# Performance work log

Measured on AMD Instinct MI355X. Metric: run time of the kernel, lower is better.

## Reference

```python
import jax, jax.numpy as jnp
import numpy as np

CHUNK = 2048  # query chunk for KNN to avoid materializing full NxN distance matrix


def _knn_single(pos, k):
    # pos: [N,3] -> idx [N,k] of k nearest neighbors (incl. self)
    N = pos.shape[0]
    qs = pos.reshape(N // CHUNK, CHUNK, 3)

    def per_chunk(q):
        d = jnp.sum((q[:, None, :] - pos[None, :, :]) ** 2, axis=-1)  # [CHUNK,N]
        _, idx = jax.lax.top_k(-d, k)
        return idx

    return jax.lax.map(per_chunk, qs).reshape(N, k)


def setup_inputs() -> dict:
    key = jax.random.key(0)
    ks = jax.random.split(key, 8)
    B, N, Cin, Cout, H, K = 2, 16384, 32, 64, 128, 16
    Ein = 2 * Cin + 3  # in_feat + out(self)_feat + rel_pos

    def lin(k_, fi, fo):
        return jax.random.normal(k_, (fi, fo), jnp.float32) / np.sqrt(fi)

    return dict(
        positions=jax.random.uniform(ks[0], (B, N, 3), jnp.float32),
        features=jax.random.normal(ks[1], (B, N, Cin), jnp.float32),
        W1=lin(ks[2], Ein, H), b1=jnp.zeros((H,), jnp.float32),
        W2=lin(ks[3], H, Cout), b2=jnp.zeros((Cout,), jnp.float32),
        W3=lin(ks[4], Cout, H), b3=jnp.zeros((H,), jnp.float32),
        W4=lin(ks[5], H, Cout), b4=jnp.zeros((Cout,), jnp.float32),
        knn_k=K,
    )


def reference(positions, features, W1, b1, W2, b2, W3, b3, W4, b4, knn_k):
    # 1) KNN neighbor search per batch
    idx = jax.vmap(lambda p: _knn_single(p, knn_k))(positions)  # [B,N,K]
    gather = jax.vmap(lambda a, i: a[i])
    # 2) gather neighbor features / positions
    nbr_feat = gather(features, idx)                      # [B,N,K,Cin]
    nbr_pos = gather(positions, idx)                      # [B,N,K,3]
    rel_pos = nbr_pos - positions[:, :, None, :]          # [B,N,K,3]
    self_feat = jnp.broadcast_to(features[:, :, None, :], nbr_feat.shape)
    # 3) edge features: cat(in_feat, out_feat, rel_pos)
    edge = jnp.concatenate([nbr_feat, self_feat, rel_pos], axis=-1)  # [B,N,K,Ein]
    # 4) edge MLP
    h = jax.nn.gelu(edge @ W1 + b1) @ W2 + b2             # [B,N,K,Cout]
    # 5) mean reduction over neighbors
    agg = jnp.mean(h, axis=2)                             # [B,N,Cout]
    # 6) output MLP
    return jax.nn.gelu(agg @ W3 + b3) @ W4 + b4           # [B,N,Cout]
```

## Files before the change

### kernel.cpp

```cpp
#include <hip/hip_runtime.h>
#include <math.h>

#define N_PTS 16384
#define BATCH 2
#define CIN   32
#define H_DIM 128
#define COUT  64
#define KNN   16
#define GC    16
#define NCELL (GC * GC * GC)
#define CS    (1.0f / GC)
#define PB    4
#define CHUNK 2048

typedef unsigned short ushortT;

__device__ __forceinline__ float gelu_f(float x) {
    float x3 = x * x * x;
    float t  = tanhf(0.7978845608028654f * (x + 0.044715f * x3));
    return 0.5f * x * (1.0f + t);
}
__device__ __forceinline__ float gelu_fast(float x) {
    float z = 1.5957691216057308f * (x + 0.044715f * x * x * x);
    return x / (1.0f + __expf(-z));
}

__device__ __forceinline__ int cellco(float v) {
    int c = (int)(v * (float)GC);
    return c < 0 ? 0 : (c > GC - 1 ? GC - 1 : c);
}

__global__ __launch_bounds__(256)
void zero_kernel(int* __restrict__ cnt) {
    cnt[blockIdx.x * 256 + threadIdx.x] = 0;
}

__global__ __launch_bounds__(256)
void count_kernel(const float* __restrict__ pos, int* __restrict__ cnt) {
    const int t = blockIdx.x * 256 + threadIdx.x;
    const int b = t >> 14;
    float x = pos[(size_t)t * 3 + 0];
    float y = pos[(size_t)t * 3 + 1];
    float z = pos[(size_t)t * 3 + 2];
    int cell = (cellco(z) * GC + cellco(y)) * GC + cellco(x);
    atomicAdd(&cnt[b * NCELL + cell], 1);
}

__global__ __launch_bounds__(1024)
void scan_kernel(const int* __restrict__ cnt, int* __restrict__ off,
                 int* __restrict__ cur) {
    __shared__ int s[1024];
    const int b = blockIdx.x;
    const int t = threadIdx.x;
    const int* c = cnt + b * NCELL;
    const int base = t * 4;
    int v0 = c[base], v1 = c[base + 1], v2 = c[base + 2], v3 = c[base + 3];
    int s01 = v0 + v1, s012 = s01 + v2, tot = s012 + v3;
    s[t] = tot;
    __syncthreads();
    for (int d = 1; d < 1024; d <<= 1) {
        int add = (t >= d) ? s[t - d] : 0;
        __syncthreads();
        s[t] += add;
        __syncthreads();
    }
    int excl = s[t] - tot;
    int* ob = off + b * (NCELL + 1);
    int* cb = cur + b * NCELL;
    ob[base] = excl;            cb[base] = excl;
    ob[base + 1] = excl + v0;   cb[base + 1] = excl + v0;
    ob[base + 2] = excl + s01;  cb[base + 2] = excl + s01;
    ob[base + 3] = excl + s012; cb[base + 3] = excl + s012;
    if (t == 1023) ob[NCELL] = excl + tot;
}

__global__ __launch_bounds__(256)
void scatter_kernel(const float* __restrict__ pos, int* __restrict__ cur,
                    float4* __restrict__ pos4) {
    const int t = blockIdx.x * 256 + threadIdx.x;
    const int b = t >> 14;
    const int pid = t & (N_PTS - 1);
    float x = pos[(size_t)t * 3 + 0];
    float y = pos[(size_t)t * 3 + 1];
    float z = pos[(size_t)t * 3 + 2];
    int cell = (cellco(z) * GC + cellco(y)) * GC + cellco(x);
    int slot = atomicAdd(&cur[b * NCELL + cell], 1);
    pos4[(size_t)b * N_PTS + slot] = make_float4(x, y, z, __int_as_float(pid));
}

__global__ __launch_bounds__(64)
void knnq_kernel(const float4* __restrict__ pos4,
                 const int* __restrict__ off, ushortT* __restrict__ out_idx) {
    const int t = blockIdx.x * 64 + threadIdx.x;
    const int b = t >> 14;
    const float4 Q = pos4[t];
    const float qx = Q.x, qy = Q.y, qz = Q.z;
    const int pid = __float_as_int(Q.w);
    const int cx = cellco(qx), cy = cellco(qy), cz = cellco(qz);
    const float4* p4b = pos4 + (size_t)b * N_PTS;
    const int* offb = off + b * (NCELL + 1);

    float ld[KNN]; int li[KNN];
#pragma unroll
    for (int p = 0; p < KNN; ++p) { ld[p] = 3.0e38f; li[p] = 0x7fffffff; }
    float t15d = 3.0e38f; int t15i = 0x7fffffff;

    auto scan_range = [&](int s, int e2) {
        for (int u = s; u < e2; u += 8) {
            float4 pg[8];
#pragma unroll
            for (int i = 0; i < 8; ++i) {
                int uu = u + i; uu = uu < e2 - 1 ? uu : e2 - 1;
                pg[i] = p4b[uu];
            }
#pragma unroll
            for (int i = 0; i < 8; ++i) {
                if (u + i >= e2) break;
                float ddx = __fsub_rn(qx, pg[i].x);
                float ddy = __fsub_rn(qy, pg[i].y);
                float ddz = __fsub_rn(qz, pg[i].z);
                float d = __fadd_rn(__fadd_rn(__fmul_rn(ddx, ddx),
                                              __fmul_rn(ddy, ddy)),
                                    __fmul_rn(ddz, ddz));
                int pj = __float_as_int(pg[i].w);
                if (d < t15d || (d == t15d && pj < t15i)) {
                    float cd = d; int cj = pj;
#pragma unroll
                    for (int p = 0; p < KNN; ++p) {
                        bool sw = (cd < ld[p]) || (cd == ld[p] && cj < li[p]);
                        float td = ld[p]; int ti = li[p];
                        ld[p] = sw ? cd : td; li[p] = sw ? cj : ti;
                        cd = sw ? td : cd;    cj = sw ? ti : cj;
                    }
                    t15d = ld[KNN - 1]; t15i = li[KNN - 1];
                }
            }
        }
    };

    for (int r = 1; r <= GC; ++r) {
        for (int dz = -r; dz <= r; ++dz) {
            const int Z = cz + dz; if ((unsigned)Z >= GC) continue;
            for (int dy = -r; dy <= r; ++dy) {
                const int Y = cy + dy; if ((unsigned)Y >= GC) continue;
                const int rowbase = (Z * GC + Y) * GC;
                const bool fullrow = (r == 1) ||
                    (dz == -r || dz == r || dy == -r || dy == r);
                if (fullrow) {
                    int X0 = cx - r; X0 = X0 < 0 ? 0 : X0;
                    int X1 = cx + r; X1 = X1 > GC - 1 ? GC - 1 : X1;
                    scan_range(offb[rowbase + X0], offb[rowbase + X1 + 1]);
                } else {
                    const int Xl = cx - r, Xr = cx + r;
                    if (Xl >= 0)
                        scan_range(offb[rowbase + Xl], offb[rowbase + Xl + 1]);
                    if (Xr <= GC - 1)
                        scan_range(offb[rowbase + Xr], offb[rowbase + Xr + 1]);
                }
            }
        }
        float mg = 1.0e19f;
        if (cx - r > 0)      mg = fminf(mg, qx - (float)(cx - r) * CS);
        if (cx + r < GC - 1) mg = fminf(mg, (float)(cx + r + 1) * CS - qx);
        if (cy - r > 0)      mg = fminf(mg, qy - (float)(cy - r) * CS);
        if (cy + r < GC - 1) mg = fminf(mg, (float)(cy + r + 1) * CS - qy);
        if (cz - r > 0)      mg = fminf(mg, qz - (float)(cz - r) * CS);
        if (cz + r < GC - 1) mg = fminf(mg, (float)(cz + r + 1) * CS - qz);
        if (t15d < mg * mg * 0.99999f) break;
    }
    ushortT* dst = out_idx + ((size_t)(b << 14) + pid) * KNN;
#pragma unroll
    for (int p = 0; p < KNN; ++p) dst[p] = (ushortT)li[p];
}

__global__ __launch_bounds__(256)
void feat1_kernel(const float* __restrict__ feats, const float* __restrict__ W1,
                  float* __restrict__ feat1) {
    const int g = blockIdx.x * 256 + threadIdx.x;
    const int p = g >> 7;
    const int h = g & 127;
    const float* fr = feats + (size_t)p * CIN;
    float a = 0.f;
#pragma unroll
    for (int c = 0; c < CIN; ++c)
        a += fr[c] * W1[c * H_DIM + h];
    feat1[g] = a;
}

__global__ __launch_bounds__(64)
void mlp2_kernel(const float* __restrict__ pos, const float* __restrict__ feats,
                 const ushortT* __restrict__ knn_idx, const float* __restrict__ feat1,
                 const float* __restrict__ W1, const float* __restrict__ b1,
                 const float* __restrict__ W2, const float* __restrict__ b2,
                 const float* __restrict__ W3, const float* __restrict__ b3,
                 const float* __restrict__ W4, const float* __restrict__ b4,
                 float* __restrict__ out) {
    __shared__ ushortT sIdx[PB][KNN];
    __shared__ float sq[PB][3];
    __shared__ __align__(16) float fself[PB][CIN];
    __shared__ float npx[PB][KNN][3];
    __shared__ __align__(16) float gs[PB][H_DIM];
    __shared__ __align__(16) float aggs[PB][COUT];
    __shared__ __align__(16) float hs[PB][H_DIM];

    const int tid = threadIdx.x;
    const int h0 = tid, h1 = tid + 64;
    const int i0 = blockIdx.x * PB;
    const size_t bofs = (size_t)(i0 >> 14) * N_PTS;

    for (int e = tid; e < PB * KNN; e += 64)
        sIdx[e >> 4][e & 15] = knn_idx[(size_t)(i0 + (e >> 4)) * KNN + (e & 15)];
    for (int e = tid; e < PB * 3; e += 64)
        sq[e / 3][e % 3] = pos[(size_t)(i0 + e / 3) * 3 + (e % 3)];
    for (int e = tid; e < PB * CIN; e += 64)
        fself[e >> 5][e & 31] = feats[(size_t)(i0 + (e >> 5)) * CIN + (e & 31)];
    __syncthreads();
    for (int e = tid; e < PB * KNN * 3; e += 64) {
        int p = e / (KNN * 3), r = e % (KNN * 3), k = r / 3, c = r % 3;
        npx[p][k][c] = pos[(bofs + sIdx[p][k]) * 3 + c];
    }

    const float w0A = W1[(2 * CIN + 0) * H_DIM + h0], w0B = W1[(2 * CIN + 0) * H_DIM + h1];
    const float w1A = W1[(2 * CIN + 1) * H_DIM + h0], w1B = W1[(2 * CIN + 1) * H_DIM + h1];
    const float w2A = W1[(2 * CIN + 2) * H_DIM + h0], w2B = W1[(2 * CIN + 2) * H_DIM + h1];
    float bA[PB], bB[PB];
#pragma unroll
    for (int p = 0; p < PB; ++p) { bA[p] = b1[h0]; bB[p] = b1[h1]; }
    __syncthreads();
#pragma unroll
    for (int c = 0; c < CIN; ++c) {
        float wA = W1[(CIN + c) * H_DIM + h0];
        float wB = W1[(CIN + c) * H_DIM + h1];
#pragma unroll
        for (int p = 0; p < PB; ++p) {
            bA[p] += fself[p][c] * wA;
            bB[p] += fself[p][c] * wB;
        }
    }

    float accA[PB] = {0.f, 0.f, 0.f, 0.f};
    float accB[PB] = {0.f, 0.f, 0.f, 0.f};
    for (int k = 0; k < KNN; ++k) {
#pragma unroll
        for (int p = 0; p < PB; ++p) {
            const float* fr = feat1 + (bofs + sIdx[p][k]) * H_DIM;
            float rx = npx[p][k][0] - sq[p][0];
            float ry = npx[p][k][1] - sq[p][1];
            float rz = npx[p][k][2] - sq[p][2];
            float uA = bA[p] + fr[h0] + rx * w0A + ry * w1A + rz * w2A;
            float uB = bB[p] + fr[h1] + rx * w0B + ry * w1B + rz * w2B;
            accA[p] += gelu_fast(uA);
            accB[p] += gelu_fast(uB);
        }
    }
#pragma unroll
    for (int p = 0; p < PB; ++p) {
        gs[p][h0] = accA[p] * (1.0f / KNN);
        gs[p][h1] = accB[p] * (1.0f / KNN);
    }
    __syncthreads();

    float a2[PB];
#pragma unroll
    for (int p = 0; p < PB; ++p) a2[p] = b2[h0];
    for (int c4 = 0; c4 < H_DIM / 4; ++c4) {
        float wx = W2[(4 * c4 + 0) * COUT + h0];
        float wy = W2[(4 * c4 + 1) * COUT + h0];
        float wz = W2[(4 * c4 + 2) * COUT + h0];
        float ww = W2[(4 * c4 + 3) * COUT + h0];
#pragma unroll
        for (int p = 0; p < PB; ++p) {
            float4 g = ((const float4*)gs[p])[c4];
            a2[p] += g.x * wx + g.y * wy + g.z * wz + g.w * ww;
        }
    }
#pragma unroll
    for (int p = 0; p < PB; ++p) aggs[p][h0] = a2[p];
    __syncthreads();

    float a3A[PB], a3B[PB];
#pragma unroll
    for (int p = 0; p < PB; ++p) { a3A[p] = b3[h0]; a3B[p] = b3[h1]; }
    for (int c4 = 0; c4 < COUT / 4; ++c4) {
        float wxA = W3[(4 * c4 + 0) * H_DIM + h0], wxB = W3[(4 * c4 + 0) * H_DIM + h1];
        float wyA = W3[(4 * c4 + 1) * H_DIM + h0], wyB = W3[(4 * c4 + 1) * H_DIM + h1];
        float wzA = W3[(4 * c4 + 2) * H_DIM + h0], wzB = W3[(4 * c4 + 2) * H_DIM + h1];
        float wwA = W3[(4 * c4 + 3) * H_DIM + h0], wwB = W3[(4 * c4 + 3) * H_DIM + h1];
#pragma unroll
        for (int p = 0; p < PB; ++p) {
            float4 g = ((const float4*)aggs[p])[c4];
            a3A[p] += g.x * wxA + g.y * wyA + g.z * wzA + g.w * wwA;
            a3B[p] += g.x * wxB + g.y * wyB + g.z * wzB + g.w * wwB;
        }
    }
#pragma unroll
    for (int p = 0; p < PB; ++p) {
        hs[p][h0] = gelu_fast(a3A[p]);
        hs[p][h1] = gelu_fast(a3B[p]);
    }
    __syncthreads();

    float o4[PB];
#pragma unroll
    for (int p = 0; p < PB; ++p) o4[p] = b4[h0];
    for (int c4 = 0; c4 < H_DIM / 4; ++c4) {
        float wx = W4[(4 * c4 + 0) * COUT + h0];
        float wy = W4[(4 * c4 + 1) * COUT + h0];
        float wz = W4[(4 * c4 + 2) * COUT + h0];
        float ww = W4[(4 * c4 + 3) * COUT + h0];
#pragma unroll
        for (int p = 0; p < PB; ++p) {
            float4 v = ((const float4*)hs[p])[c4];
            o4[p] += v.x * wx + v.y * wy + v.z * wz + v.w * ww;
        }
    }
#pragma unroll
    for (int p = 0; p < PB; ++p)
        out[(size_t)(i0 + p) * COUT + h0] = o4[p];
}

__global__ __launch_bounds__(64)
void mlp_kernel(const float* __restrict__ pos, const float* __restrict__ feats,
                const ushortT* __restrict__ knn_idx,
                const float* __restrict__ W1, const float* __restrict__ b1,
                const float* __restrict__ W2, const float* __restrict__ b2,
                const float* __restrict__ W3, const float* __restrict__ b3,
                const float* __restrict__ W4, const float* __restrict__ b4,
                float* __restrict__ out) {
    __shared__ ushortT sIdx[PB][KNN];
    __shared__ float sq[PB][3];
    __shared__ __align__(16) float fself[PB][CIN];
    __shared__ float npx[PB][KNN][3];
    __shared__ __align__(16) float nf[PB][KNN][CIN];
    __shared__ __align__(16) float gs[PB][H_DIM];
    __shared__ __align__(16) float aggs[PB][COUT];
    __shared__ __align__(16) float hs[PB][H_DIM];

    const int tid = threadIdx.x;
    const int h0 = tid, h1 = tid + 64;
    const int i0 = blockIdx.x * PB;
    const size_t bofs = (size_t)(i0 >> 14) * N_PTS;

    for (int e = tid; e < PB * KNN; e += 64)
        sIdx[e >> 4][e & 15] = knn_idx[(size_t)(i0 + (e >> 4)) * KNN + (e & 15)];
    for (int e = tid; e < PB * 3; e += 64)
        sq[e / 3][e % 3] = pos[(size_t)(i0 + e / 3) * 3 + (e % 3)];
    for (int e = tid; e < PB * CIN; e += 64)
        fself[e >> 5][e & 31] = feats[(size_t)(i0 + (e >> 5)) * CIN + (e & 31)];
    __syncthreads();
    for (int e = tid; e < PB * KNN * CIN; e += 64) {
        int p = e >> 9, k = (e >> 5) & 15, c = e & 31;
        nf[p][k][c] = feats[(bofs + sIdx[p][k]) * CIN + c];
    }
    for (int e = tid; e < PB * KNN * 3; e += 64) {
        int p = e / (KNN * 3), r = e % (KNN * 3), k = r / 3, c = r % 3;
        npx[p][k][c] = pos[(bofs + sIdx[p][k]) * 3 + c];
    }

    float w1rA[CIN], w1rB[CIN];
#pragma unroll
    for (int c = 0; c < CIN; ++c) {
        w1rA[c] = W1[c * H_DIM + h0];
        w1rB[c] = W1[c * H_DIM + h1];
    }
    const float w0A = W1[(2 * CIN + 0) * H_DIM + h0], w0B = W1[(2 * CIN + 0) * H_DIM + h1];
    const float w1A = W1[(2 * CIN + 1) * H_DIM + h0], w1B = W1[(2 * CIN + 1) * H_DIM + h1];
    const float w2A = W1[(2 * CIN + 2) * H_DIM + h0], w2B = W1[(2 * CIN + 2) * H_DIM + h1];
    float bA[PB], bB[PB];
#pragma unroll
    for (int p = 0; p < PB; ++p) { bA[p] = b1[h0]; bB[p] = b1[h1]; }
    __syncthreads();
#pragma unroll
    for (int c = 0; c < CIN; ++c) {
        float wA = W1[(CIN + c) * H_DIM + h0];
        float wB = W1[(CIN + c) * H_DIM + h1];
#pragma unroll
        for (int p = 0; p < PB; ++p) {
            bA[p] += fself[p][c] * wA;
            bB[p] += fself[p][c] * wB;
        }
    }

    float accA[PB] = {0.f, 0.f, 0.f, 0.f};
    float accB[PB] = {0.f, 0.f, 0.f, 0.f};
    for (int k = 0; k < KNN; ++k) {
#pragma unroll
        for (int p = 0; p < PB; ++p) {
            float rx = npx[p][k][0] - sq[p][0];
            float ry = npx[p][k][1] - sq[p][1];
            float rz = npx[p][k][2] - sq[p][2];
            float uA = bA[p] + rx * w0A + ry * w1A + rz * w2A;
            float uB = bB[p] + rx * w0B + ry * w1B + rz * w2B;
            const float4* nf4 = (const float4*)nf[p][k];
#pragma unroll
            for (int c4 = 0; c4 < CIN / 4; ++c4) {
                float4 v = nf4[c4];
                uA += v.x * w1rA[4 * c4] + v.y * w1rA[4 * c4 + 1]
                    + v.z * w1rA[4 * c4 + 2] + v.w * w1rA[4 * c4 + 3];
                uB += v.x * w1rB[4 * c4] + v.y * w1rB[4 * c4 + 1]
                    + v.z * w1rB[4 * c4 + 2] + v.w * w1rB[4 * c4 + 3];
            }
            accA[p] += gelu_f(uA);
            accB[p] += gelu_f(uB);
        }
    }
#pragma unroll
    for (int p = 0; p < PB; ++p) {
        gs[p][h0] = accA[p] * (1.0f / KNN);
        gs[p][h1] = accB[p] * (1.0f / KNN);
    }
    __syncthreads();

    float a2[PB];
#pragma unroll
    for (int p = 0; p < PB; ++p) a2[p] = b2[h0];
    for (int c4 = 0; c4 < H_DIM / 4; ++c4) {
        float wx = W2[(4 * c4 + 0) * COUT + h0];
        float wy = W2[(4 * c4 + 1) * COUT + h0];
        float wz = W2[(4 * c4 + 2) * COUT + h0];
        float ww = W2[(4 * c4 + 3) * COUT + h0];
#pragma unroll
        for (int p = 0; p < PB; ++p) {
            float4 g = ((const float4*)gs[p])[c4];
            a2[p] += g.x * wx + g.y * wy + g.z * wz + g.w * ww;
        }
    }
#pragma unroll
    for (int p = 0; p < PB; ++p) aggs[p][h0] = a2[p];
    __syncthreads();

    float a3A[PB], a3B[PB];
#pragma unroll
    for (int p = 0; p < PB; ++p) { a3A[p] = b3[h0]; a3B[p] = b3[h1]; }
    for (int c4 = 0; c4 < COUT / 4; ++c4) {
        float wxA = W3[(4 * c4 + 0) * H_DIM + h0], wxB = W3[(4 * c4 + 0) * H_DIM + h1];
        float wyA = W3[(4 * c4 + 1) * H_DIM + h0], wyB = W3[(4 * c4 + 1) * H_DIM + h1];
        float wzA = W3[(4 * c4 + 2) * H_DIM + h0], wzB = W3[(4 * c4 + 2) * H_DIM + h1];
        float wwA = W3[(4 * c4 + 3) * H_DIM + h0], wwB = W3[(4 * c4 + 3) * H_DIM + h1];
#pragma unroll
        for (int p = 0; p < PB; ++p) {
            float4 g = ((const float4*)aggs[p])[c4];
            a3A[p] += g.x * wxA + g.y * wyA + g.z * wzA + g.w * wwA;
            a3B[p] += g.x * wxB + g.y * wyB + g.z * wzB + g.w * wwB;
        }
    }
#pragma unroll
    for (int p = 0; p < PB; ++p) {
        hs[p][h0] = gelu_f(a3A[p]);
        hs[p][h1] = gelu_f(a3B[p]);
    }
    __syncthreads();

    float o4[PB];
#pragma unroll
    for (int p = 0; p < PB; ++p) o4[p] = b4[h0];
    for (int c4 = 0; c4 < H_DIM / 4; ++c4) {
        float wx = W4[(4 * c4 + 0) * COUT + h0];
        float wy = W4[(4 * c4 + 1) * COUT + h0];
        float wz = W4[(4 * c4 + 2) * COUT + h0];
        float ww = W4[(4 * c4 + 3) * COUT + h0];
#pragma unroll
        for (int p = 0; p < PB; ++p) {
            float4 v = ((const float4*)hs[p])[c4];
            o4[p] += v.x * wx + v.y * wy + v.z * wz + v.w * ww;
        }
    }
#pragma unroll
    for (int p = 0; p < PB; ++p)
        out[(size_t)(i0 + p) * COUT + h0] = o4[p];
}

#define NT    128
#define LP    17
__global__ __launch_bounds__(NT)
void fused_kernel(const float* __restrict__ pos, const float* __restrict__ feats,
                  const float* __restrict__ W1, const float* __restrict__ b1,
                  const float* __restrict__ W2, const float* __restrict__ b2,
                  const float* __restrict__ W3, const float* __restrict__ b3,
                  const float* __restrict__ W4, const float* __restrict__ b4,
                  float* __restrict__ out) {
    __shared__ float sx[CHUNK], sy[CHUNK], sz[CHUNK];
    __shared__ float ld0[NT * LP]; __shared__ int li0[NT * LP];
    __shared__ float ld1[NT * LP]; __shared__ int li1[NT * LP];
    __shared__ int   sIdx[KNN];
    __shared__ float npx[KNN][3];
    __shared__ float nf[KNN][CIN];
    __shared__ float fself[CIN];
    __shared__ float gs[H_DIM];
    __shared__ float aggs[COUT];
    __shared__ float hs[H_DIM];

    const int i   = blockIdx.x;
    const int b   = i >> 14;
    const int tid = threadIdx.x;
    const float* posb = pos + (size_t)b * N_PTS * 3;

    const float qx = pos[(size_t)i * 3 + 0];
    const float qy = pos[(size_t)i * 3 + 1];
    const float qz = pos[(size_t)i * 3 + 2];

    const int base = tid * LP;
    for (int s = 0; s < KNN; ++s) { ld0[base + s] = 3.0e38f; li0[base + s] = 0x7fffffff; }
    float taild = 3.0e38f;

    for (int cbase = 0; cbase < N_PTS; cbase += CHUNK) {
        __syncthreads();
        for (int t = tid; t < CHUNK * 3; t += NT) {
            float v = posb[(size_t)cbase * 3 + t];
            int c = t % 3, r = t / 3;
            (c == 0 ? sx : (c == 1 ? sy : sz))[r] = v;
        }
        __syncthreads();
        for (int r = tid; r < CHUNK; r += NT) {
            float dx = __fsub_rn(qx, sx[r]);
            float dy = __fsub_rn(qy, sy[r]);
            float dz = __fsub_rn(qz, sz[r]);
            float d  = __fadd_rn(__fadd_rn(__fmul_rn(dx, dx), __fmul_rn(dy, dy)),
                                 __fmul_rn(dz, dz));
            const int j = cbase + r;
            if (d < taild) {
                int p = KNN - 1;
                while (p > 0) {
                    float pd = ld0[base + p - 1];
                    if (!(pd > d)) break;
                    ld0[base + p] = pd;
                    li0[base + p] = li0[base + p - 1];
                    --p;
                }
                ld0[base + p] = d;
                li0[base + p] = j;
                taild = ld0[base + KNN - 1];
            }
        }
    }

    int cur = 0;
    for (int s = 1; s < NT; s <<= 1) {
        __syncthreads();
        if ((tid & (2 * s - 1)) == 0) {
            const float* cd  = cur ? ld1 : ld0;
            const int*   cix = cur ? li1 : li0;
            float* nd  = cur ? ld0 : ld1;
            int*   nix = cur ? li0 : li1;
            const int A = tid * LP, B = (tid + s) * LP, O = tid * LP;
            int a = 0, bb = 0;
            for (int o = 0; o < KNN; ++o) {
                float da = cd[A + a], db = cd[B + bb];
                int   ia = cix[A + a], ib = cix[B + bb];
                bool tA = (da < db) || (da == db && ia < ib);
                nd[O + o]  = tA ? da : db;
                nix[O + o] = tA ? ia : ib;
                a += tA ? 1 : 0; bb += tA ? 0 : 1;
            }
        }
        cur ^= 1;
    }
    __syncthreads();
    {
        const int* fli = cur ? li1 : li0;
        if (tid < KNN) sIdx[tid] = fli[tid];
        if (tid < CIN) fself[tid] = feats[(size_t)i * CIN + tid];
    }
    __syncthreads();

    for (int e = tid; e < KNN * CIN; e += NT) {
        int k = e >> 5, c = e & 31;
        nf[k][c] = feats[((size_t)b * N_PTS + sIdx[k]) * CIN + c];
    }
    if (tid < KNN * 3) {
        int k = tid / 3, c = tid % 3;
        npx[k][c] = posb[sIdx[k] * 3 + c];
    }
    const int h = tid;
    float w1r[CIN];
#pragma unroll
    for (int c = 0; c < CIN; ++c) w1r[c] = W1[c * H_DIM + h];
    float baseh = b1[h];
    const float w0 = W1[(2 * CIN + 0) * H_DIM + h];
    const float w1 = W1[(2 * CIN + 1) * H_DIM + h];
    const float w2 = W1[(2 * CIN + 2) * H_DIM + h];
#pragma unroll
    for (int c = 0; c < CIN; ++c)
        baseh += fself[c] * W1[(CIN + c) * H_DIM + h];
    __syncthreads();

    float acc = 0.f;
    for (int k = 0; k < KNN; ++k) {
        float u = baseh
                + (npx[k][0] - qx) * w0
                + (npx[k][1] - qy) * w1
                + (npx[k][2] - qz) * w2;
#pragma unroll
        for (int c = 0; c < CIN; ++c)
            u += nf[k][c] * w1r[c];
        acc += gelu_f(u);
    }
    gs[h] = acc * (1.0f / KNN);
    __syncthreads();

    if (h < COUT) {
        float a = b2[h];
#pragma unroll
        for (int t2 = 0; t2 < H_DIM; ++t2)
            a += gs[t2] * W2[t2 * COUT + h];
        aggs[h] = a;
    }
    __syncthreads();

    float a3 = b3[h];
#pragma unroll
    for (int c = 0; c < COUT; ++c)
        a3 += aggs[c] * W3[c * H_DIM + h];
    hs[h] = gelu_f(a3);
    __syncthreads();
    if (h < COUT) {
        float o = b4[h];
#pragma unroll
        for (int t2 = 0; t2 < H_DIM; ++t2)
            o += hs[t2] * W4[t2 * COUT + h];
        out[(size_t)i * COUT + h] = o;
    }
}

extern "C" void kernel_launch(void* const* d_in, const int* in_sizes, int n_in,
                              void* d_out, int out_size, void* d_ws, size_t ws_size,
                              hipStream_t stream) {
    const float* pos   = (const float*)d_in[0];
    const float* feats = (const float*)d_in[1];
    const float* W1    = (const float*)d_in[2];
    const float* b1    = (const float*)d_in[3];
    const float* W2    = (const float*)d_in[4];
    const float* b2    = (const float*)d_in[5];
    const float* W3    = (const float*)d_in[6];
    const float* b3    = (const float*)d_in[7];
    const float* W4    = (const float*)d_in[8];
    const float* b4    = (const float*)d_in[9];
    float* out = (float*)d_out;

    const int M = BATCH * N_PTS;

    char* ws = (char*)d_ws;
    const size_t need_small = (size_t)1536 * 1024 + 97 * 1024;
    const size_t need_big   = (size_t)18 * 1024 * 1024;

    if (ws_size >= need_small && d_ws != nullptr) {
        ushortT* idx  = (ushortT*)ws;
        float4*  pos4 = (float4*)(ws + (size_t)1024 * 1024);
        int*     cnt  = (int*)(ws + (size_t)1536 * 1024);
        int*     off  = (int*)(ws + (size_t)1536 * 1024 + 32 * 1024);
        int*     curp = (int*)(ws + (size_t)1536 * 1024 + 65 * 1024);

        zero_kernel   <<<(BATCH * NCELL) / 256, 256, 0, stream>>>(cnt);
        count_kernel  <<<M / 256, 256, 0, stream>>>(pos, cnt);
        scan_kernel   <<<BATCH, 1024, 0, stream>>>(cnt, off, curp);
        scatter_kernel<<<M / 256, 256, 0, stream>>>(pos, curp, pos4);
        knnq_kernel   <<<M / 64, 64, 0, stream>>>(pos4, off, idx);

        if (ws_size >= need_big) {
            float* feat1 = (float*)(ws + (size_t)2 * 1024 * 1024);
            feat1_kernel<<<(M * H_DIM) / 256, 256, 0, stream>>>(feats, W1, feat1);
            mlp2_kernel <<<M / PB, 64, 0, stream>>>(pos, feats, idx, feat1,
                                                    W1, b1, W2, b2, W3, b3, W4, b4, out);
        } else {
            mlp_kernel  <<<M / PB, 64, 0, stream>>>(pos, feats, idx,
                                                    W1, b1, W2, b2, W3, b3, W4, b4, out);
        }
    } else {
        fused_kernel<<<M, NT, 0, stream>>>(pos, feats, W1, b1, W2, b2,
                                           W3, b3, W4, b4, out);
    }
}
```

Before: 388.6 us.

## Split each KNN query across four lanes with shared pruning threshold and merge

The grid KNN kernel now assigns four threads per query, each scanning a strided subset of the cell rows in every ring. After each ring the per-lane 16th-best distances are combined in shared memory into a tighter shared pruning bound, and the block stops once all 16 queries satisfy the ring-distance termination test. At the end the four partial top-16 lists are merged by one thread per query. This gives four times as many threads, improving latency hiding and occupancy. In exchange it adds three block barriers per ring, lockstep rings across queries, and a serial merge.

Result: slower. 477.4 us (+22.9%).

```diff
diff --git a/kernel.cpp b/kernel.cpp
--- a/kernel.cpp
+++ b/kernel.cpp
@@ -11,6 +11,7 @@
 #define NCELL (GC * GC * GC)
 #define CS    (1.0f / GC)
 #define PB    4
+#define QPB2  16
 #define CHUNK 2048
 
 typedef unsigned short ushortT;
@@ -89,13 +90,24 @@
 }
 
 __global__ __launch_bounds__(64)
-void knnq_kernel(const float4* __restrict__ pos4,
-                 const int* __restrict__ off, ushortT* __restrict__ out_idx) {
-    const int t = blockIdx.x * 64 + threadIdx.x;
-    const int b = t >> 14;
+void knnq4_kernel(const float4* __restrict__ pos4,
+                  const int* __restrict__ off, ushortT* __restrict__ out_idx) {
+    __shared__ float m4d[QPB2][4];
+    __shared__ int   m4i[QPB2][4];
+    __shared__ float taud_s[QPB2];
+    __shared__ int   taui_s[QPB2];
+    __shared__ int   sflag[QPB2];
+    __shared__ int   sAll;
+    __shared__ float sd[QPB2][4][KNN];
+    __shared__ int   si[QPB2][4][KNN];
+
+    const int tid  = threadIdx.x;
+    const int qloc = tid >> 2;
+    const int w    = tid & 3;
+    const int t    = blockIdx.x * QPB2 + qloc;
+    const int b    = t >> 14;
     const float4 Q = pos4[t];
     const float qx = Q.x, qy = Q.y, qz = Q.z;
-    const int pid = __float_as_int(Q.w);
     const int cx = cellco(qx), cy = cellco(qy), cz = cellco(qz);
     const float4* p4b = pos4 + (size_t)b * N_PTS;
     const int* offb = off + b * (NCELL + 1);
@@ -104,6 +116,8 @@
 #pragma unroll
     for (int p = 0; p < KNN; ++p) { ld[p] = 3.0e38f; li[p] = 0x7fffffff; }
     float t15d = 3.0e38f; int t15i = 0x7fffffff;
+    float taud = 3.0e38f; int taui = 0x7fffffff;
+    bool qdone = false;
 
     auto scan_range = [&](int s, int e2) {
         for (int u = s; u < e2; u += 8) {
@@ -123,7 +137,9 @@
                                               __fmul_rn(ddy, ddy)),
                                     __fmul_rn(ddz, ddz));
                 int pj = __float_as_int(pg[i].w);
-                if (d < t15d || (d == t15d && pj < t15i)) {
+                bool accOwn = (d < t15d) || (d == t15d && pj < t15i);
+                bool accSh  = (d < taud) || (d == taud && pj < taui);
+                if (accOwn && accSh) {
                     float cd = d; int cj = pj;
 #pragma unroll
                     for (int p = 0; p < KNN; ++p) {
@@ -139,38 +155,89 @@
     };
 
     for (int r = 1; r <= GC; ++r) {
-        for (int dz = -r; dz <= r; ++dz) {
-            const int Z = cz + dz; if ((unsigned)Z >= GC) continue;
-            for (int dy = -r; dy <= r; ++dy) {
-                const int Y = cy + dy; if ((unsigned)Y >= GC) continue;
-                const int rowbase = (Z * GC + Y) * GC;
-                const bool fullrow = (r == 1) ||
-                    (dz == -r || dz == r || dy == -r || dy == r);
-                if (fullrow) {
-                    int X0 = cx - r; X0 = X0 < 0 ? 0 : X0;
-                    int X1 = cx + r; X1 = X1 > GC - 1 ? GC - 1 : X1;
-                    scan_range(offb[rowbase + X0], offb[rowbase + X1 + 1]);
-                } else {
-                    const int Xl = cx - r, Xr = cx + r;
-                    if (Xl >= 0)
-                        scan_range(offb[rowbase + Xl], offb[rowbase + Xl + 1]);
-                    if (Xr <= GC - 1)
-                        scan_range(offb[rowbase + Xr], offb[rowbase + Xr + 1]);
+        if (!qdone) {
+            int ccnt = 0;
+            for (int dz = -r; dz <= r; ++dz) {
+                const int Z = cz + dz; if ((unsigned)Z >= GC) continue;
+                for (int dy = -r; dy <= r; ++dy) {
+                    const int Y = cy + dy; if ((unsigned)Y >= GC) continue;
+                    const int rowbase = (Z * GC + Y) * GC;
+                    const bool fullrow = (r == 1) ||
+                        (dz == -r || dz == r || dy == -r || dy == r);
+                    if (fullrow) {
+                        if (((ccnt++) & 3) == w) {
+                            int X0 = cx - r; X0 = X0 < 0 ? 0 : X0;
+                            int X1 = cx + r; X1 = X1 > GC - 1 ? GC - 1 : X1;
+                            scan_range(offb[rowbase + X0], offb[rowbase + X1 + 1]);
+                        }
+                    } else {
+                        const int Xl = cx - r, Xr = cx + r;
+                        if (Xl >= 0) {
+                            if (((ccnt++) & 3) == w)
+                                scan_range(offb[rowbase + Xl], offb[rowbase + Xl + 1]);
+                        }
+                        if (Xr <= GC - 1) {
+                            if (((ccnt++) & 3) == w)
+                                scan_range(offb[rowbase + Xr], offb[rowbase + Xr + 1]);
+                        }
+                    }
                 }
             }
         }
-        float mg = 1.0e19f;
-        if (cx - r > 0)      mg = fminf(mg, qx - (float)(cx - r) * CS);
-        if (cx + r < GC - 1) mg = fminf(mg, (float)(cx + r + 1) * CS - qx);
-        if (cy - r > 0)      mg = fminf(mg, qy - (float)(cy - r) * CS);
-        if (cy + r < GC - 1) mg = fminf(mg, (float)(cy + r + 1) * CS - qy);
-        if (cz - r > 0)      mg = fminf(mg, qz - (float)(cz - r) * CS);
-        if (cz + r < GC - 1) mg = fminf(mg, (float)(cz + r + 1) * CS - qz);
-        if (t15d < mg * mg * 0.99999f) break;
-    }
-    ushortT* dst = out_idx + ((size_t)(b << 14) + pid) * KNN;
-#pragma unroll
-    for (int p = 0; p < KNN; ++p) dst[p] = (ushortT)li[p];
+        m4d[qloc][w] = t15d; m4i[qloc][w] = t15i;
+        __syncthreads();
+        if (w == 0) {
+            float bd = m4d[qloc][0]; int bi = m4i[qloc][0];
+#pragma unroll
+            for (int w2 = 1; w2 < 4; ++w2) {
+                float d2 = m4d[qloc][w2]; int i2 = m4i[qloc][w2];
+                if (d2 < bd || (d2 == bd && i2 < bi)) { bd = d2; bi = i2; }
+            }
+            taud_s[qloc] = bd; taui_s[qloc] = bi;
+            float mg = 1.0e19f;
+            if (cx - r > 0)      mg = fminf(mg, qx - (float)(cx - r) * CS);
+            if (cx + r < GC - 1) mg = fminf(mg, (float)(cx + r + 1) * CS - qx);
+            if (cy - r > 0)      mg = fminf(mg, qy - (float)(cy - r) * CS);
+            if (cy + r < GC - 1) mg = fminf(mg, (float)(cy + r + 1) * CS - qy);
+            if (cz - r > 0)      mg = fminf(mg, qz - (float)(cz - r) * CS);
+            if (cz + r < GC - 1) mg = fminf(mg, (float)(cz + r + 1) * CS - qz);
+            sflag[qloc] = (bd < mg * mg * 0.99999f) ? 1 : 0;
+        }
+        __syncthreads();
+        if (tid == 0) {
+            int sacc = 0;
+            for (int j = 0; j < QPB2; ++j) sacc += sflag[j];
+            sAll = sacc;
+        }
+        __syncthreads();
+        taud = taud_s[qloc]; taui = taui_s[qloc];
+        qdone = sflag[qloc] != 0;
+        if (sAll == QPB2) break;
+    }
+
+#pragma unroll
+    for (int p = 0; p < KNN; ++p) { sd[qloc][w][p] = ld[p]; si[qloc][w][p] = li[p]; }
+    __syncthreads();
+    if (tid < QPB2) {
+        int hp[4] = {0, 0, 0, 0};
+        const int ts = blockIdx.x * QPB2 + tid;
+        const int bq = ts >> 14;
+        const int pidq = __float_as_int(pos4[ts].w);
+        ushortT* dst = out_idx + ((size_t)(bq << 14) + pidq) * KNN;
+        for (int o = 0; o < KNN; ++o) {
+            float bd = 3.4e38f; int bi = 0x7fffffff; int bw = 0;
+#pragma unroll
+            for (int w2 = 0; w2 < 4; ++w2) {
+                int p2 = hp[w2];
+                if (p2 < KNN) {
+                    float d2 = sd[tid][w2][p2]; int i2 = si[tid][w2][p2];
+                    if (d2 < bd || (d2 == bd && i2 < bi)) { bd = d2; bi = i2; bw = w2; }
+                }
+            }
+            hp[bw]++;
+            dst[o] = (ushortT)bi;
+        }
+    }
 }
 
 __global__ __launch_bounds__(256)
@@ -654,7 +721,7 @@
         count_kernel  <<<M / 256, 256, 0, stream>>>(pos, cnt);
         scan_kernel   <<<BATCH, 1024, 0, stream>>>(cnt, off, curp);
         scatter_kernel<<<M / 256, 256, 0, stream>>>(pos, curp, pos4);
-        knnq_kernel   <<<M / 64, 64, 0, stream>>>(pos4, off, idx);
+        knnq4_kernel  <<<M / QPB2, 64, 0, stream>>>(pos4, off, idx);
 
         if (ws_size >= need_big) {
             float* feat1 = (float*)(ws + (size_t)2 * 1024 * 1024);
```

## Stage neighbouring grid-cell points in LDS for KNN query blocks

Applied to the files above, without the earlier changes.

Each 64-query block computes the Z/Y cell extent of its queries, expands it by two cells (capped at 7x7 rows), and cooperatively copies those full X-rows of sorted points into a shared-memory buffer of up to 2560 float4. Candidate scans then read from LDS when the row was staged and fall back to global loads otherwise. This targets repeated global/L2 traffic from many queries scanning the same cells. In exchange it adds several block barriers, serial per-block setup done by one thread, about 40KB of LDS per 64-thread block (which limits occupancy), and per-point LDS reads without batching.

Measured after the change: 422.7 us. +8.8%, slower.

```diff
diff --git a/kernel.cpp b/kernel.cpp
--- a/kernel.cpp
+++ b/kernel.cpp
@@ -12,6 +12,8 @@
 #define CS    (1.0f / GC)
 #define PB    4
 #define CHUNK 2048
+#define ROWCAP 49
+#define PTCAP  2560
 
 typedef unsigned short ushortT;
 
@@ -91,7 +93,15 @@
 __global__ __launch_bounds__(64)
 void knnq_kernel(const float4* __restrict__ pos4,
                  const int* __restrict__ off, ushortT* __restrict__ out_idx) {
-    const int t = blockIdx.x * 64 + threadIdx.x;
+    __shared__ int zy[128];
+    __shared__ int win[5];
+    __shared__ int tblS[ROWCAP];
+    __shared__ int tblC[ROWCAP];
+    __shared__ int tblB[ROWCAP];
+    __shared__ __align__(16) float4 lpt[PTCAP];
+
+    const int tid = threadIdx.x;
+    const int t = blockIdx.x * 64 + tid;
     const int b = t >> 14;
     const float4 Q = pos4[t];
     const float qx = Q.x, qy = Q.y, qz = Q.z;
@@ -100,39 +110,112 @@
     const float4* p4b = pos4 + (size_t)b * N_PTS;
     const int* offb = off + b * (NCELL + 1);
 
+    zy[tid] = cz; zy[64 + tid] = cy;
+    __syncthreads();
+    if (tid == 0) {
+        int Zl = zy[0], Zh = zy[0], Yl = zy[64], Yh = zy[64];
+        for (int i = 1; i < 64; ++i) {
+            int z2 = zy[i], y2 = zy[64 + i];
+            Zl = z2 < Zl ? z2 : Zl;  Zh = z2 > Zh ? z2 : Zh;
+            Yl = y2 < Yl ? y2 : Yl;  Yh = y2 > Yh ? y2 : Yh;
+        }
+        int Zc0 = Zl - 2 < 0 ? 0 : Zl - 2;
+        int Zc1 = Zh + 2 > GC - 1 ? GC - 1 : Zh + 2;
+        int Yc0 = Yl - 2 < 0 ? 0 : Yl - 2;
+        int Yc1 = Yh + 2 > GC - 1 ? GC - 1 : Yh + 2;
+        if (Zc1 - Zc0 + 1 > 7) Zc1 = Zc0 + 6;
+        if (Yc1 - Yc0 + 1 > 7) Yc1 = Yc0 + 6;
+        win[0] = Zc0; win[1] = Zc1 - Zc0 + 1;
+        win[2] = Yc0; win[3] = Yc1 - Yc0 + 1;
+        win[4] = win[1] * win[3];
+    }
+    __syncthreads();
+    const int Zc0 = win[0], NZc = win[1], Yc0 = win[2], NYc = win[3];
+    const int nrows = win[4];
+    if (tid < nrows) {
+        int Z = Zc0 + tid / NYc, Y = Yc0 + tid % NYc;
+        int rowbase = (Z * GC + Y) * GC;
+        int s = offb[rowbase], e = offb[rowbase + GC];
+        tblS[tid] = s; tblC[tid] = e - s;
+    }
+    __syncthreads();
+    if (tid == 0) {
+        int base = 0;
+        for (int i = 0; i < nrows; ++i) {
+            int c = tblC[i];
+            if (base + c <= PTCAP) { tblB[i] = base; base += c; }
+            else tblB[i] = -1;
+        }
+    }
+    __syncthreads();
+    for (int i = 0; i < nrows; ++i) {
+        int bse = tblB[i];
+        if (bse >= 0) {
+            int s = tblS[i], c = tblC[i];
+            for (int j = tid; j < c; j += 64) lpt[bse + j] = p4b[s + j];
+        }
+    }
+    __syncthreads();
+
     float ld[KNN]; int li[KNN];
 #pragma unroll
     for (int p = 0; p < KNN; ++p) { ld[p] = 3.0e38f; li[p] = 0x7fffffff; }
     float t15d = 3.0e38f; int t15i = 0x7fffffff;
 
-    auto scan_range = [&](int s, int e2) {
-        for (int u = s; u < e2; u += 8) {
-            float4 pg[8];
-#pragma unroll
-            for (int i = 0; i < 8; ++i) {
-                int uu = u + i; uu = uu < e2 - 1 ? uu : e2 - 1;
-                pg[i] = p4b[uu];
+    auto insert_cand = [&](float d, int pj) {
+        if (d < t15d || (d == t15d && pj < t15i)) {
+            float cd = d; int cj = pj;
+#pragma unroll
+            for (int p = 0; p < KNN; ++p) {
+                bool sw = (cd < ld[p]) || (cd == ld[p] && cj < li[p]);
+                float td = ld[p]; int ti = li[p];
+                ld[p] = sw ? cd : td; li[p] = sw ? cj : ti;
+                cd = sw ? td : cd;    cj = sw ? ti : cj;
             }
-#pragma unroll
-            for (int i = 0; i < 8; ++i) {
-                if (u + i >= e2) break;
-                float ddx = __fsub_rn(qx, pg[i].x);
-                float ddy = __fsub_rn(qy, pg[i].y);
-                float ddz = __fsub_rn(qz, pg[i].z);
+            t15d = ld[KNN - 1]; t15i = li[KNN - 1];
+        }
+    };
+
+    auto scan_row = [&](int Z, int Y, int X0, int X1) {
+        const int rowbase = (Z * GC + Y) * GC;
+        const int s = offb[rowbase + X0], e2 = offb[rowbase + X1 + 1];
+        const int rz = Z - Zc0, ry = Y - Yc0;
+        bool inLds = false; int o = 0;
+        if (rz >= 0 && rz < NZc && ry >= 0 && ry < NYc) {
+            const int ri = rz * NYc + ry;
+            const int bse = tblB[ri];
+            if (bse >= 0) { inLds = true; o = bse + (s - tblS[ri]); }
+        }
+        if (inLds) {
+            const int n = e2 - s;
+            for (int u = 0; u < n; ++u) {
+                float4 P = lpt[o + u];
+                float ddx = __fsub_rn(qx, P.x);
+                float ddy = __fsub_rn(qy, P.y);
+                float ddz = __fsub_rn(qz, P.z);
                 float d = __fadd_rn(__fadd_rn(__fmul_rn(ddx, ddx),
                                               __fmul_rn(ddy, ddy)),
                                     __fmul_rn(ddz, ddz));
-                int pj = __float_as_int(pg[i].w);
-                if (d < t15d || (d == t15d && pj < t15i)) {
-                    float cd = d; int cj = pj;
-#pragma unroll
-                    for (int p = 0; p < KNN; ++p) {
-                        bool sw = (cd < ld[p]) || (cd == ld[p] && cj < li[p]);
-                        float td = ld[p]; int ti = li[p];
-                        ld[p] = sw ? cd : td; li[p] = sw ? cj : ti;
-                        cd = sw ? td : cd;    cj = sw ? ti : cj;
-                    }
-                    t15d = ld[KNN - 1]; t15i = li[KNN - 1];
+                insert_cand(d, __float_as_int(P.w));
+            }
+        } else {
+            for (int u = s; u < e2; u += 8) {
+                float4 pg[8];
+#pragma unroll
+                for (int i = 0; i < 8; ++i) {
+                    int uu = u + i; uu = uu < e2 - 1 ? uu : e2 - 1;
+                    pg[i] = p4b[uu];
+                }
+#pragma unroll
+                for (int i = 0; i < 8; ++i) {
+                    if (u + i >= e2) break;
+                    float ddx = __fsub_rn(qx, pg[i].x);
+                    float ddy = __fsub_rn(qy, pg[i].y);
+                    float ddz = __fsub_rn(qz, pg[i].z);
+                    float d = __fadd_rn(__fadd_rn(__fmul_rn(ddx, ddx),
+                                                  __fmul_rn(ddy, ddy)),
+                                        __fmul_rn(ddz, ddz));
+                    insert_cand(d, __float_as_int(pg[i].w));
                 }
             }
         }
@@ -143,19 +226,16 @@
             const int Z = cz + dz; if ((unsigned)Z >= GC) continue;
             for (int dy = -r; dy <= r; ++dy) {
                 const int Y = cy + dy; if ((unsigned)Y >= GC) continue;
-                const int rowbase = (Z * GC + Y) * GC;
                 const bool fullrow = (r == 1) ||
                     (dz == -r || dz == r || dy == -r || dy == r);
                 if (fullrow) {
                     int X0 = cx - r; X0 = X0 < 0 ? 0 : X0;
                     int X1 = cx + r; X1 = X1 > GC - 1 ? GC - 1 : X1;
-                    scan_range(offb[rowbase + X0], offb[rowbase + X1 + 1]);
+                    scan_row(Z, Y, X0, X1);
                 } else {
                     const int Xl = cx - r, Xr = cx + r;
-                    if (Xl >= 0)
-                        scan_range(offb[rowbase + Xl], offb[rowbase + Xl + 1]);
-                    if (Xr <= GC - 1)
-                        scan_range(offb[rowbase + Xr], offb[rowbase + Xr + 1]);
+                    if (Xl >= 0)      scan_row(Z, Y, Xl, Xl);
+                    if (Xr <= GC - 1) scan_row(Z, Y, Xr, Xr);
                 }
             }
         }
```

## Split each KNN query across 16 lanes with shared-memory top-k merge

Applied to the files above, without the earlier changes.

The grid KNN search now assigns 16 threads to each query instead of one. Each lane scans a strided subset of the candidate points and keeps its own top-16 list. After each ring of cells, the lanes share a global threshold (the best per-lane 16th distance) to prune candidates. At the end the per-lane lists are combined with a two-level 4-way merge in shared memory. This targets the serial per-thread scan and its divergence, at the cost of block-wide syncs on every ring, extra shared memory, and a merge done by a few lanes only.

Measured after the change: 536.6 us. +38.1%, slower.

```diff
diff --git a/kernel.cpp b/kernel.cpp
--- a/kernel.cpp
+++ b/kernel.cpp
@@ -88,14 +88,27 @@
     pos4[(size_t)b * N_PTS + slot] = make_float4(x, y, z, __int_as_float(pid));
 }
 
-__global__ __launch_bounds__(64)
-void knnq_kernel(const float4* __restrict__ pos4,
-                 const int* __restrict__ off, ushortT* __restrict__ out_idx) {
-    const int t = blockIdx.x * 64 + threadIdx.x;
-    const int b = t >> 14;
+__global__ __launch_bounds__(256)
+void knnq16_kernel(const float4* __restrict__ pos4,
+                   const int* __restrict__ off, ushortT* __restrict__ out_idx) {
+    __shared__ float   bufD[16][16][16];
+    __shared__ ushortT bufI[16][16][16];
+    __shared__ float   b4D[16][4][16];
+    __shared__ ushortT b4I[16][4][16];
+    __shared__ float   rd16[16][16];
+    __shared__ int     ri16[16][16];
+    __shared__ float   taud_s[16];
+    __shared__ int     taui_s[16];
+    __shared__ int     sflag[16];
+    __shared__ int     sAll;
+
+    const int tid  = threadIdx.x;
+    const int q    = tid >> 4;
+    const int lane = tid & 15;
+    const int t    = blockIdx.x * 16 + q;
+    const int b    = t >> 14;
     const float4 Q = pos4[t];
     const float qx = Q.x, qy = Q.y, qz = Q.z;
-    const int pid = __float_as_int(Q.w);
     const int cx = cellco(qx), cy = cellco(qy), cz = cellco(qz);
     const float4* p4b = pos4 + (size_t)b * N_PTS;
     const int* offb = off + b * (NCELL + 1);
@@ -104,73 +117,132 @@
 #pragma unroll
     for (int p = 0; p < KNN; ++p) { ld[p] = 3.0e38f; li[p] = 0x7fffffff; }
     float t15d = 3.0e38f; int t15i = 0x7fffffff;
-
-    auto scan_range = [&](int s, int e2) {
-        for (int u = s; u < e2; u += 8) {
-            float4 pg[8];
-#pragma unroll
-            for (int i = 0; i < 8; ++i) {
-                int uu = u + i; uu = uu < e2 - 1 ? uu : e2 - 1;
-                pg[i] = p4b[uu];
+    float taud = 3.0e38f; int taui = 0x7fffffff;
+    bool qdone = false;
+
+    auto scan_row = [&](int rowbase, int X0, int X1) {
+        const int s = offb[rowbase + X0], e2 = offb[rowbase + X1 + 1];
+        for (int u = s + lane; u < e2; u += 16) {
+            float4 P = p4b[u];
+            float ddx = __fsub_rn(qx, P.x);
+            float ddy = __fsub_rn(qy, P.y);
+            float ddz = __fsub_rn(qz, P.z);
+            float d = __fadd_rn(__fadd_rn(__fmul_rn(ddx, ddx),
+                                          __fmul_rn(ddy, ddy)),
+                                __fmul_rn(ddz, ddz));
+            int pj = __float_as_int(P.w);
+            bool acc = ((d < t15d) || (d == t15d && pj < t15i)) &&
+                       ((d < taud) || (d == taud && pj < taui));
+            if (acc) {
+                float cd = d; int cj = pj;
+#pragma unroll
+                for (int p = 0; p < KNN; ++p) {
+                    bool sw = (cd < ld[p]) || (cd == ld[p] && cj < li[p]);
+                    float td = ld[p]; int ti = li[p];
+                    ld[p] = sw ? cd : td; li[p] = sw ? cj : ti;
+                    cd = sw ? td : cd;    cj = sw ? ti : cj;
+                }
+                t15d = ld[KNN - 1]; t15i = li[KNN - 1];
             }
-#pragma unroll
-            for (int i = 0; i < 8; ++i) {
-                if (u + i >= e2) break;
-                float ddx = __fsub_rn(qx, pg[i].x);
-                float ddy = __fsub_rn(qy, pg[i].y);
-                float ddz = __fsub_rn(qz, pg[i].z);
-                float d = __fadd_rn(__fadd_rn(__fmul_rn(ddx, ddx),
-                                              __fmul_rn(ddy, ddy)),
-                                    __fmul_rn(ddz, ddz));
-                int pj = __float_as_int(pg[i].w);
-                if (d < t15d || (d == t15d && pj < t15i)) {
-                    float cd = d; int cj = pj;
-#pragma unroll
-                    for (int p = 0; p < KNN; ++p) {
-                        bool sw = (cd < ld[p]) || (cd == ld[p] && cj < li[p]);
-                        float td = ld[p]; int ti = li[p];
-                        ld[p] = sw ? cd : td; li[p] = sw ? cj : ti;
-                        cd = sw ? td : cd;    cj = sw ? ti : cj;
+        }
+    };
+
+    for (int r = 1; r <= GC; ++r) {
+        if (!qdone) {
+            for (int dz = -r; dz <= r; ++dz) {
+                const int Z = cz + dz; if ((unsigned)Z >= GC) continue;
+                for (int dy = -r; dy <= r; ++dy) {
+                    const int Y = cy + dy; if ((unsigned)Y >= GC) continue;
+                    const int rowbase = (Z * GC + Y) * GC;
+                    const bool fullrow = (r == 1) ||
+                        (dz == -r || dz == r || dy == -r || dy == r);
+                    if (fullrow) {
+                        int X0 = cx - r; X0 = X0 < 0 ? 0 : X0;
+                        int X1 = cx + r; X1 = X1 > GC - 1 ? GC - 1 : X1;
+                        scan_row(rowbase, X0, X1);
+                    } else {
+                        const int Xl = cx - r, Xr = cx + r;
+                        if (Xl >= 0)      scan_row(rowbase, Xl, Xl);
+                        if (Xr <= GC - 1) scan_row(rowbase, Xr, Xr);
                     }
-                    t15d = ld[KNN - 1]; t15i = li[KNN - 1];
                 }
             }
         }
-    };
-
-    for (int r = 1; r <= GC; ++r) {
-        for (int dz = -r; dz <= r; ++dz) {
-            const int Z = cz + dz; if ((unsigned)Z >= GC) continue;
-            for (int dy = -r; dy <= r; ++dy) {
-                const int Y = cy + dy; if ((unsigned)Y >= GC) continue;
-                const int rowbase = (Z * GC + Y) * GC;
-                const bool fullrow = (r == 1) ||
-                    (dz == -r || dz == r || dy == -r || dy == r);
-                if (fullrow) {
-                    int X0 = cx - r; X0 = X0 < 0 ? 0 : X0;
-                    int X1 = cx + r; X1 = X1 > GC - 1 ? GC - 1 : X1;
-                    scan_range(offb[rowbase + X0], offb[rowbase + X1 + 1]);
-                } else {
-                    const int Xl = cx - r, Xr = cx + r;
-                    if (Xl >= 0)
-                        scan_range(offb[rowbase + Xl], offb[rowbase + Xl + 1]);
-                    if (Xr <= GC - 1)
-                        scan_range(offb[rowbase + Xr], offb[rowbase + Xr + 1]);
+        rd16[q][lane] = t15d; ri16[q][lane] = t15i;
+        __syncthreads();
+        if (lane == 0) {
+            float bd = rd16[q][0]; int bi = ri16[q][0];
+#pragma unroll
+            for (int l2 = 1; l2 < 16; ++l2) {
+                float d2 = rd16[q][l2]; int i2 = ri16[q][l2];
+                if (d2 < bd || (d2 == bd && i2 < bi)) { bd = d2; bi = i2; }
+            }
+            taud_s[q] = bd; taui_s[q] = bi;
+            float mg = 1.0e19f;
+            if (cx - r > 0)      mg = fminf(mg, qx - (float)(cx - r) * CS);
+            if (cx + r < GC - 1) mg = fminf(mg, (float)(cx + r + 1) * CS - qx);
+            if (cy - r > 0)      mg = fminf(mg, qy - (float)(cy - r) * CS);
+            if (cy + r < GC - 1) mg = fminf(mg, (float)(cy + r + 1) * CS - qy);
+            if (cz - r > 0)      mg = fminf(mg, qz - (float)(cz - r) * CS);
+            if (cz + r < GC - 1) mg = fminf(mg, (float)(cz + r + 1) * CS - qz);
+            sflag[q] = (bd < mg * mg * 0.99999f) ? 1 : 0;
+        }
+        __syncthreads();
+        if (tid == 0) {
+            int sacc = 0;
+            for (int j = 0; j < 16; ++j) sacc += sflag[j];
+            sAll = sacc;
+        }
+        __syncthreads();
+        taud = taud_s[q]; taui = taui_s[q];
+        qdone = sflag[q] != 0;
+        if (sAll == 16) break;
+    }
+
+#pragma unroll
+    for (int p = 0; p < KNN; ++p) {
+        bufD[q][lane][p] = ld[p];
+        bufI[q][lane][p] = (ushortT)li[p];
+    }
+    __syncthreads();
+
+    if (lane < 4) {
+        const int lb = lane * 4;
+        int hp[4] = {0, 0, 0, 0};
+        for (int o = 0; o < KNN; ++o) {
+            float bd = 3.4e38f; int bi = 0x7fffffff; int bw = 0;
+#pragma unroll
+            for (int w2 = 0; w2 < 4; ++w2) {
+                if (hp[w2] < KNN) {
+                    float d2 = bufD[q][lb + w2][hp[w2]];
+                    int   i2 = (int)bufI[q][lb + w2][hp[w2]];
+                    if (d2 < bd || (d2 == bd && i2 < bi)) { bd = d2; bi = i2; bw = w2; }
                 }
             }
-        }
-        float mg = 1.0e19f;
-        if (cx - r > 0)      mg = fminf(mg, qx - (float)(cx - r) * CS);
-        if (cx + r < GC - 1) mg = fminf(mg, (float)(cx + r + 1) * CS - qx);
-        if (cy - r > 0)      mg = fminf(mg, qy - (float)(cy - r) * CS);
-        if (cy + r < GC - 1) mg = fminf(mg, (float)(cy + r + 1) * CS - qy);
-        if (cz - r > 0)      mg = fminf(mg, qz - (float)(cz - r) * CS);
-        if (cz + r < GC - 1) mg = fminf(mg, (float)(cz + r + 1) * CS - qz);
-        if (t15d < mg * mg * 0.99999f) break;
-    }
-    ushortT* dst = out_idx + ((size_t)(b << 14) + pid) * KNN;
-#pragma unroll
-    for (int p = 0; p < KNN; ++p) dst[p] = (ushortT)li[p];
+            hp[bw]++;
+            b4D[q][lane][o] = bd; b4I[q][lane][o] = (ushortT)bi;
+        }
+    }
+    __syncthreads();
+
+    if (lane == 0) {
+        int hp[4] = {0, 0, 0, 0};
+        const int pid = __float_as_int(Q.w);
+        ushortT* dst = out_idx + ((size_t)(b << 14) + pid) * KNN;
+        for (int o = 0; o < KNN; ++o) {
+            float bd = 3.4e38f; int bi = 0x7fffffff; int bw = 0;
+#pragma unroll
+            for (int w2 = 0; w2 < 4; ++w2) {
+                if (hp[w2] < KNN) {
+                    float d2 = b4D[q][w2][hp[w2]];
+                    int   i2 = (int)b4I[q][w2][hp[w2]];
+                    if (d2 < bd || (d2 == bd && i2 < bi)) { bd = d2; bi = i2; bw = w2; }
+                }
+            }
+            hp[bw]++;
+            dst[o] = (ushortT)bi;
+        }
+    }
 }
 
 __global__ __launch_bounds__(256)
@@ -654,7 +726,7 @@
         count_kernel  <<<M / 256, 256, 0, stream>>>(pos, cnt);
         scan_kernel   <<<BATCH, 1024, 0, stream>>>(cnt, off, curp);
         scatter_kernel<<<M / 256, 256, 0, stream>>>(pos, curp, pos4);
-        knnq_kernel   <<<M / 64, 64, 0, stream>>>(pos4, off, idx);
+        knnq16_kernel <<<M / 16, 256, 0, stream>>>(pos4, off, idx);
 
         if (ws_size >= need_big) {
             float* feat1 = (float*)(ws + (size_t)2 * 1024 * 1024);
```
